# Kernel tuning notes

Measured on AMD Instinct MI355X. Metric: run time of the kernel, lower is better.

Reference implementation:

```python
import jax, jax.numpy as jnp
import numpy as np

M, K, N = 8192, 4096, 4096
ALPHA, BETA = 0.002, 0.0005


def setup_inputs() -> dict:
    key = jax.random.key(0)
    kx, kw, kb = jax.random.split(key, 3)
    # int8-range quantized activations and weights (stored as int32 for portability)
    x = jax.random.randint(kx, (M, K), -127, 127, dtype=jnp.int32)
    weight = jax.random.randint(kw, (N, K), -127, 127, dtype=jnp.int32)  # (out, in)
    bias = jax.random.randint(kb, (1, N), -(2**20), 2**20, dtype=jnp.int32)
    alpha = jnp.float32(ALPHA)
    beta = jnp.float32(BETA)
    return {"x": x, "weight": weight, "bias": bias, "alpha": alpha, "beta": beta}


def reference(x, weight, bias, alpha, beta):
    # int8 GEMM with int32 accumulation: acc[m, n] = sum_k x[m, k] * W[n, k]
    acc = jnp.matmul(x, weight.T, preferred_element_type=jnp.int32)  # [M, N] int32
    # CUTLASS-style epilogue: D = round(alpha * acc + beta * bias) -> int32
    y = alpha * acc.astype(jnp.float32) + beta * bias.astype(jnp.float32)
    return jnp.round(y).astype(jnp.int32)
```

## Files before the change

kernel.cpp:

```cpp
#include <hip/hip_runtime.h>
#include <hip/hip_bf16.h>
#include <stdint.h>

#define M_DIM 8192
#define N_DIM 4096
#define K_DIM 4096

#define BM 256
#define BN 256
#define BK 64
#define NT (K_DIM / BK)
#define DEPTH 4

typedef int v4i __attribute__((ext_vector_type(4)));

#define AS1C(p) ((const __attribute__((address_space(1))) void*)(p))
#define AS3(p)  ((__attribute__((address_space(3))) void*)(p))

__device__ __forceinline__ int pack4(int a, int b, int c, int d) {
  return (a & 0xff) | ((b & 0xff) << 8) | ((c & 0xff) << 16) | (d << 24);
}

__global__ void pack_both_kernel(const int* __restrict__ x, const int* __restrict__ w,
                                 char* __restrict__ A8, char* __restrict__ B8,
                                 int nA, int nTot) {
  int idx = blockIdx.x * blockDim.x + threadIdx.x;
  int stride = gridDim.x * blockDim.x;
  for (int i = idx; i < nTot; i += stride) {
    const int4* pin;
    int4* pout;
    if (i < nA) {
      pin  = (const int4*)x + 4 * (size_t)i;
      pout = (int4*)A8 + i;
    } else {
      int j = i - nA;
      pin  = (const int4*)w + 4 * (size_t)j;
      pout = (int4*)B8 + j;
    }
    int4 v0 = pin[0];
    int4 v1 = pin[1];
    int4 v2 = pin[2];
    int4 v3 = pin[3];
    int4 o;
    o.x = pack4(v0.x, v0.y, v0.z, v0.w);
    o.y = pack4(v1.x, v1.y, v1.z, v1.w);
    o.z = pack4(v2.x, v2.y, v2.z, v2.w);
    o.w = pack4(v3.x, v3.y, v3.z, v3.w);
    *pout = o;
  }
}

__global__ __launch_bounds__(512, 2) void gemm_i8_kernel(
    const char* __restrict__ A8, const char* __restrict__ B8,
    const int* __restrict__ bias, const float* __restrict__ alpha_p,
    const float* __restrict__ beta_p, int* __restrict__ out) {
  __shared__ alignas(16) char lds[DEPTH][BM * BK + BN * BK];

  const int tid  = threadIdx.x;
  const int lane = tid & 63;
  const int wave = tid >> 6;

  const int orig = blockIdx.x;
  const int swz  = (orig & 7) * (512 / 8) + (orig >> 3);
  const int bm   = (swz >> 4) * BM;
  const int bn   = (swz & 15) * BN;

  int aoff[2], boff[2], ldsoff[2];
#pragma unroll
  for (int i = 0; i < 2; ++i) {
    int linear = i * 8192 + tid * 16;
    int row = linear >> 6;
    int p   = (linear >> 4) & 3;
    int g   = p ^ ((row >> 1) & 3);
    ldsoff[i] = i * 8192 + wave * 1024;
    aoff[i] = (bm + row) * K_DIM + g * 16;
    boff[i] = (bn + row) * K_DIM + g * 16;
  }

#define STAGE_A(t)                                                                  \
  do {                                                                              \
    const char* ab_ = A8 + (size_t)(t) * BK;                                        \
    char* base_ = &lds[(t) & (DEPTH - 1)][0];                                       \
    _Pragma("unroll") for (int i_ = 0; i_ < 2; ++i_)                                \
      __builtin_amdgcn_global_load_lds(AS1C(ab_ + aoff[i_]),                        \
                                       AS3(base_ + ldsoff[i_]), 16, 0, 0);          \
  } while (0)

#define STAGE_B(t)                                                                  \
  do {                                                                              \
    const char* bb_ = B8 + (size_t)(t) * BK;                                        \
    char* base_ = &lds[(t) & (DEPTH - 1)][0];                                       \
    _Pragma("unroll") for (int i_ = 0; i_ < 2; ++i_)                                \
      __builtin_amdgcn_global_load_lds(AS1C(bb_ + boff[i_]),                        \
                                       AS3(base_ + 16384 + ldsoff[i_]), 16, 0, 0);  \
  } while (0)

  v4i acc[8][4];
#pragma unroll
  for (int i = 0; i < 8; ++i)
#pragma unroll
    for (int j = 0; j < 4; ++j) acc[i][j] = (v4i){0, 0, 0, 0};

  const int wr = wave >> 2;
  const int wc = wave & 3;
  const int frow = lane & 15;
  const int fchunk = lane >> 4;
  const int swzoff = ((fchunk ^ ((frow >> 1) & 3)) << 4);

  v4i bf0[4], aflo0[4], bf1[4], aflo1[4], afhi[4];

#define READ0(S, t)                                                                 \
  do {                                                                              \
    const char* base_ = &lds[(t) & (DEPTH - 1)][0];                                 \
    _Pragma("unroll") for (int nj = 0; nj < 4; ++nj)                                \
      bf##S[nj] = *(const v4i*)(base_ + 16384 + (wc * 64 + nj * 16 + frow) * 64 +   \
                                swzoff);                                            \
    _Pragma("unroll") for (int mi = 0; mi < 4; ++mi)                                \
      aflo##S[mi] = *(const v4i*)(base_ + (wr * 128 + mi * 16 + frow) * 64 +        \
                                  swzoff);                                          \
  } while (0)

#define READ1(t)                                                                    \
  do {                                                                              \
    const char* base_ = &lds[(t) & (DEPTH - 1)][0];                                 \
    _Pragma("unroll") for (int mi = 0; mi < 4; ++mi)                                \
      afhi[mi] = *(const v4i*)(base_ + (wr * 128 + (mi + 4) * 16 + frow) * 64 +     \
                               swzoff);                                             \
  } while (0)

#define MFMA_LO(S)                                                                  \
  do {                                                                              \
    __builtin_amdgcn_s_setprio(1);                                                  \
    _Pragma("unroll") for (int mi = 0; mi < 4; ++mi)                                \
      _Pragma("unroll") for (int nj = 0; nj < 4; ++nj)                              \
        acc[mi][nj] = __builtin_amdgcn_mfma_i32_16x16x64_i8(aflo##S[mi], bf##S[nj], \
                                                            acc[mi][nj], 0, 0, 0); \
    __builtin_amdgcn_s_setprio(0);                                                  \
  } while (0)

#define MFMA_HI(S)                                                                  \
  do {                                                                              \
    __builtin_amdgcn_s_setprio(1);                                                  \
    _Pragma("unroll") for (int mi = 0; mi < 4; ++mi)                                \
      _Pragma("unroll") for (int nj = 0; nj < 4; ++nj)                              \
        acc[mi + 4][nj] = __builtin_amdgcn_mfma_i32_16x16x64_i8(afhi[mi], bf##S[nj],\
                                                                acc[mi + 4][nj],   \
                                                                0, 0, 0);          \
    __builtin_amdgcn_s_setprio(0);                                                  \
  } while (0)

#define EVWAIT(EV)                                                                  \
  do {                                                                              \
    if ((EV) == 4) asm volatile("s_waitcnt vmcnt(4)" ::: "memory");                 \
    if ((EV) == 0) asm volatile("s_waitcnt vmcnt(0)" ::: "memory");                 \
    if ((EV) >= 0) __builtin_amdgcn_s_barrier();                                    \
  } while (0)

#define TILE_E(t, C, N, STG, EV)                                                    \
  do {                                                                              \
    if (STG) STAGE_A((t) + 3);                                                      \
    READ1(t);                                                                       \
    MFMA_LO(C);                                                                     \
    if (STG) STAGE_B((t) + 3);                                                      \
    if ((t) + 1 < NT) READ0(N, (t) + 1);                                            \
    MFMA_HI(C);                                                                     \
    EVWAIT(EV);                                                                     \
  } while (0)

#define TILE_O(t, C, N, STG, EV)                                                    \
  do {                                                                              \
    MFMA_LO(C);                                                                     \
    if (STG) STAGE_A((t) + 3);                                                      \
    READ1(t);                                                                       \
    MFMA_HI(C);                                                                     \
    if (STG) STAGE_B((t) + 3);                                                      \
    if ((t) + 1 < NT) READ0(N, (t) + 1);                                            \
    EVWAIT(EV);                                                                     \
  } while (0)

  STAGE_A(0); STAGE_B(0);
  STAGE_A(1); STAGE_B(1);
  STAGE_A(2); STAGE_B(2);
  asm volatile("s_waitcnt vmcnt(4)" ::: "memory");
  __builtin_amdgcn_s_barrier();
  READ0(0, 0);

  if ((wave & 4) == 0) {
    for (int t = 0; t < NT - 4; t += 2) {
      TILE_E(t, 0, 1, true, 4);
      TILE_E(t + 1, 1, 0, true, 4);
    }
    TILE_E(NT - 4, 0, 1, true, 4);
    TILE_E(NT - 3, 1, 0, false, 0);
    TILE_E(NT - 2, 0, 1, false, -1);
    TILE_E(NT - 1, 1, 0, false, -1);
  } else {
    for (int t = 0; t < NT - 4; t += 2) {
      TILE_O(t, 0, 1, true, 4);
      TILE_O(t + 1, 1, 0, true, 4);
    }
    TILE_O(NT - 4, 0, 1, true, 4);
    TILE_O(NT - 3, 1, 0, false, 0);
    TILE_O(NT - 2, 0, 1, false, -1);
    TILE_O(NT - 1, 1, 0, false, -1);
  }

  const float alpha = *alpha_p;
  const float beta  = *beta_p;
  const int col0 = bn + wc * 64 + frow;
  float bb4[4];
#pragma unroll
  for (int nj = 0; nj < 4; ++nj) bb4[nj] = beta * (float)bias[col0 + nj * 16];

  const int rbase = bm + wr * 128 + (lane >> 4) * 4;
#pragma unroll
  for (int mi = 0; mi < 8; ++mi) {
#pragma unroll
    for (int r = 0; r < 4; ++r) {
      size_t rowoff = (size_t)(rbase + mi * 16 + r) * N_DIM;
#pragma unroll
      for (int nj = 0; nj < 4; ++nj) {
        out[rowoff + col0 + nj * 16] =
            (int)rintf(fmaf(alpha, (float)acc[mi][nj][r], bb4[nj]));
      }
    }
  }
#undef STAGE_A
#undef STAGE_B
#undef READ0
#undef READ1
#undef MFMA_LO
#undef MFMA_HI
#undef EVWAIT
#undef TILE_E
#undef TILE_O
}

__global__ void naive_kernel(const int* __restrict__ x, const int* __restrict__ w,
                             const int* __restrict__ bias,
                             const float* __restrict__ alpha_p,
                             const float* __restrict__ beta_p,
                             int* __restrict__ out) {
  size_t idx = (size_t)blockIdx.x * 256 + threadIdx.x;
  int m = (int)(idx / N_DIM);
  int n = (int)(idx % N_DIM);
  const int4* xr = (const int4*)(x + (size_t)m * K_DIM);
  const int4* wr = (const int4*)(w + (size_t)n * K_DIM);
  int acc = 0;
  for (int k = 0; k < K_DIM / 4; ++k) {
    int4 a = xr[k];
    int4 b = wr[k];
    acc += a.x * b.x + a.y * b.y + a.z * b.z + a.w * b.w;
  }
  out[idx] = (int)rintf(fmaf(*alpha_p, (float)acc, (*beta_p) * (float)bias[n]));
}

extern "C" void kernel_launch(void* const* d_in, const int* in_sizes, int n_in,
                              void* d_out, int out_size, void* d_ws, size_t ws_size,
                              hipStream_t stream) {
  const int*   x     = (const int*)d_in[0];
  const int*   w     = (const int*)d_in[1];
  const int*   bias  = (const int*)d_in[2];
  const float* alpha = (const float*)d_in[3];
  const float* beta  = (const float*)d_in[4];
  int* out = (int*)d_out;

  const size_t a8_bytes = (size_t)M_DIM * K_DIM;
  const size_t b8_bytes = (size_t)N_DIM * K_DIM;

  if (ws_size >= a8_bytes + b8_bytes) {
    char* A8 = (char*)d_ws;
    char* B8 = A8 + a8_bytes;
    const int nA = (int)(a8_bytes / 16);
    const int nTot = (int)((a8_bytes + b8_bytes) / 16);
    pack_both_kernel<<<2048, 256, 0, stream>>>(x, w, A8, B8, nA, nTot);
    const int nblk = (M_DIM / BM) * (N_DIM / BN);
    gemm_i8_kernel<<<nblk, 512, 0, stream>>>(A8, B8, bias, alpha, beta, out);
  } else {
    naive_kernel<<<(M_DIM * (size_t)N_DIM) / 256, 256, 0, stream>>>(x, w, bias, alpha, beta, out);
  }
}
```

Before: 180.5 us.

## Make GEMM blocks compute two M-tiles each, overlapping epilogue with next prefetch

```diff
diff --git a/kernel.cpp b/kernel.cpp
--- a/kernel.cpp
+++ b/kernel.cpp
@@ -11,6 +11,7 @@
 #define BK 64
 #define NT (K_DIM / BK)
 #define DEPTH 4
+#define RND_DELTA (16 * BM * K_DIM)
 
 typedef int v4i __attribute__((ext_vector_type(4)));
 
@@ -61,9 +62,10 @@
   const int wave = tid >> 6;
 
   const int orig = blockIdx.x;
-  const int swz  = (orig & 7) * (512 / 8) + (orig >> 3);
-  const int bm   = (swz >> 4) * BM;
-  const int bn   = (swz & 15) * BN;
+  const int xcd  = orig & 7;
+  const int j    = orig >> 3;
+  const int bn   = (xcd * 2 + (j >> 4)) * BN;
+  int       bm   = (j & 15) * BM;
 
   int aoff[2], boff[2], ldsoff[2];
 #pragma unroll
@@ -99,7 +101,7 @@
 #pragma unroll
   for (int i = 0; i < 8; ++i)
 #pragma unroll
-    for (int j = 0; j < 4; ++j) acc[i][j] = (v4i){0, 0, 0, 0};
+    for (int jj = 0; jj < 4; ++jj) acc[i][jj] = (v4i){0, 0, 0, 0};
 
   const int wr = wave >> 2;
   const int wc = wave & 3;
@@ -178,6 +180,37 @@
     EVWAIT(EV);                                                                     \
   } while (0)
 
+#define KLOOP_E()                                                                   \
+  do {                                                                              \
+    for (int t = 0; t < NT - 4; t += 2) {                                           \
+      TILE_E(t, 0, 1, true, 4);                                                     \
+      TILE_E(t + 1, 1, 0, true, 4);                                                 \
+    }                                                                               \
+    TILE_E(NT - 4, 0, 1, true, 4);                                                  \
+    TILE_E(NT - 3, 1, 0, false, 0);                                                 \
+    TILE_E(NT - 2, 0, 1, false, -1);                                                \
+    TILE_E(NT - 1, 1, 0, false, -1);                                                \
+  } while (0)
+
+#define KLOOP_O()                                                                   \
+  do {                                                                              \
+    for (int t = 0; t < NT - 4; t += 2) {                                           \
+      TILE_O(t, 0, 1, true, 4);                                                     \
+      TILE_O(t + 1, 1, 0, true, 4);                                                 \
+    }                                                                               \
+    TILE_O(NT - 4, 0, 1, true, 4);                                                  \
+    TILE_O(NT - 3, 1, 0, false, 0);                                                 \
+    TILE_O(NT - 2, 0, 1, false, -1);                                                \
+    TILE_O(NT - 1, 1, 0, false, -1);                                                \
+  } while (0)
+
+  const float alpha = *alpha_p;
+  const float beta  = *beta_p;
+  const int col0 = bn + wc * 64 + frow;
+  float bb4[4];
+#pragma unroll
+  for (int nj = 0; nj < 4; ++nj) bb4[nj] = beta * (float)bias[col0 + nj * 16];
+
   STAGE_A(0); STAGE_B(0);
   STAGE_A(1); STAGE_B(1);
   STAGE_A(2); STAGE_B(2);
@@ -185,44 +218,45 @@
   __builtin_amdgcn_s_barrier();
   READ0(0, 0);
 
-  if ((wave & 4) == 0) {
-    for (int t = 0; t < NT - 4; t += 2) {
-      TILE_E(t, 0, 1, true, 4);
-      TILE_E(t + 1, 1, 0, true, 4);
+#pragma unroll 1
+  for (int rnd = 0; rnd < 2; ++rnd) {
+    if ((wave & 4) == 0) KLOOP_E();
+    else                 KLOOP_O();
+
+    if (rnd == 0) {
+      __builtin_amdgcn_s_barrier();
+      aoff[0] += RND_DELTA;
+      aoff[1] += RND_DELTA;
+      STAGE_A(0); STAGE_B(0);
+      STAGE_A(1); STAGE_B(1);
+      STAGE_A(2); STAGE_B(2);
     }
-    TILE_E(NT - 4, 0, 1, true, 4);
-    TILE_E(NT - 3, 1, 0, false, 0);
-    TILE_E(NT - 2, 0, 1, false, -1);
-    TILE_E(NT - 1, 1, 0, false, -1);
-  } else {
-    for (int t = 0; t < NT - 4; t += 2) {
-      TILE_O(t, 0, 1, true, 4);
-      TILE_O(t + 1, 1, 0, true, 4);
+
+    {
+      const int rbase = bm + wr * 128 + (lane >> 4) * 4;
+#pragma unroll
+      for (int mi = 0; mi < 8; ++mi) {
+#pragma unroll
+        for (int r = 0; r < 4; ++r) {
+          size_t rowoff = (size_t)(rbase + mi * 16 + r) * N_DIM;
+#pragma unroll
+          for (int nj = 0; nj < 4; ++nj) {
+            out[rowoff + col0 + nj * 16] =
+                (int)rintf(fmaf(alpha, (float)acc[mi][nj][r], bb4[nj]));
+          }
+        }
+      }
     }
-    TILE_O(NT - 4, 0, 1, true, 4);
-    TILE_O(NT - 3, 1, 0, false, 0);
-    TILE_O(NT - 2, 0, 1, false, -1);
-    TILE_O(NT - 1, 1, 0, false, -1);
-  }
-
-  const float alpha = *alpha_p;
-  const float beta  = *beta_p;
-  const int col0 = bn + wc * 64 + frow;
-  float bb4[4];
-#pragma unroll
-  for (int nj = 0; nj < 4; ++nj) bb4[nj] = beta * (float)bias[col0 + nj * 16];
-
-  const int rbase = bm + wr * 128 + (lane >> 4) * 4;
-#pragma unroll
-  for (int mi = 0; mi < 8; ++mi) {
-#pragma unroll
-    for (int r = 0; r < 4; ++r) {
-      size_t rowoff = (size_t)(rbase + mi * 16 + r) * N_DIM;
-#pragma unroll
-      for (int nj = 0; nj < 4; ++nj) {
-        out[rowoff + col0 + nj * 16] =
-            (int)rintf(fmaf(alpha, (float)acc[mi][nj][r], bb4[nj]));
-      }
+
+    if (rnd == 0) {
+      asm volatile("s_waitcnt vmcnt(0)" ::: "memory");
+      __builtin_amdgcn_s_barrier();
+      READ0(0, 0);
+#pragma unroll
+      for (int i = 0; i < 8; ++i)
+#pragma unroll
+        for (int jj = 0; jj < 4; ++jj) acc[i][jj] = (v4i){0, 0, 0, 0};
+      bm += 16 * BM;
     }
   }
 #undef STAGE_A
@@ -234,6 +268,8 @@
 #undef EVWAIT
 #undef TILE_E
 #undef TILE_O
+#undef KLOOP_E
+#undef KLOOP_O
 }
 
 __global__ void naive_kernel(const int* __restrict__ x, const int* __restrict__ w,
@@ -274,7 +310,7 @@
     const int nA = (int)(a8_bytes / 16);
     const int nTot = (int)((a8_bytes + b8_bytes) / 16);
     pack_both_kernel<<<2048, 256, 0, stream>>>(x, w, A8, B8, nA, nTot);
-    const int nblk = (M_DIM / BM) * (N_DIM / BN);
+    const int nblk = (M_DIM / BM) * (N_DIM / BN) / 2;
     gemm_i8_kernel<<<nblk, 512, 0, stream>>>(A8, B8, bias, alpha, beta, out);
   } else {
     naive_kernel<<<(M_DIM * (size_t)N_DIM) / 256, 256, 0, stream>>>(x, w, bias, alpha, beta, out);
```

New measurement: 184.7 us. 1.02x slower.
